# Performance work log

Measured on AMD Instinct MI355X. Metric: run time of the kernel, lower is better.

## Reference

```python
import jax, jax.numpy as jnp
import numpy as np


def conv2d_same(x, w, b=None):
    # x: [B,C,H,W], w: [O,I,kh,kw], stride 1, SAME padding (pad=1 for 3x3)
    out = jax.lax.conv_general_dilated(
        x, w, window_strides=(1, 1), padding='SAME',
        dimension_numbers=('NCHW', 'OIHW', 'NCHW'))
    if b is not None:
        out = out + b[None, :, None, None]
    return out


def deform_conv(x, offset, wd, k=3, pad=1, dg=4):
    # DCNv1: per-location offset-guided bilinear sampling + weighted accumulation.
    # x: [B,C,H,W]; offset: [B, dg*k*k*2, H, W] as (dy,dx) pairs per kernel tap;
    # wd: [O, C, k, k] (bias-free, as in mmcv DeformConv).
    B, C, H, W = x.shape
    cg = C // dg          # channels per deformable group
    K = k * k
    off = offset.reshape(B, dg, K, 2, H, W)
    dy, dx = off[:, :, :, 0], off[:, :, :, 1]          # [B,dg,K,H,W]
    ky = (jnp.arange(K) // k - pad).astype(x.dtype)    # kernel row offsets
    kx = (jnp.arange(K) % k - pad).astype(x.dtype)     # kernel col offsets
    hh = jnp.arange(H, dtype=x.dtype)
    ww = jnp.arange(W, dtype=x.dtype)
    py = dy + ky[None, None, :, None, None] + hh[None, None, None, :, None]
    px = dx + kx[None, None, :, None, None] + ww[None, None, None, None, :]
    y0 = jnp.floor(py); x0 = jnp.floor(px)
    wy1 = py - y0; wy0 = 1.0 - wy1
    wx1 = px - x0; wx0 = 1.0 - wx1
    xg = x.reshape(B, dg, cg, H * W)

    def gather(yi, xi):
        # zero outside the feature map (implicit zero padding of bilinear kernel)
        valid = (yi >= 0) & (yi < H) & (xi >= 0) & (xi < W)
        yc = jnp.clip(yi, 0, H - 1).astype(jnp.int32)
        xc = jnp.clip(xi, 0, W - 1).astype(jnp.int32)
        idx = (yc * W + xc).reshape(B, dg, 1, K * H * W)
        g = jnp.take_along_axis(xg, jnp.broadcast_to(idx, (B, dg, cg, K * H * W)), axis=-1)
        g = g.reshape(B, dg, cg, K, H, W)
        return g * valid[:, :, None].astype(x.dtype)

    val = (gather(y0, x0) * (wy0 * wx0)[:, :, None]
           + gather(y0, x0 + 1) * (wy0 * wx1)[:, :, None]
           + gather(y0 + 1, x0) * (wy1 * wx0)[:, :, None]
           + gather(y0 + 1, x0 + 1) * (wy1 * wx1)[:, :, None])  # [B,dg,cg,K,H,W]
    wr = wd.reshape(wd.shape[0], dg, cg, K)
    return jnp.einsum('ogck,bgckhw->bohw', wr, val)


def setup_inputs() -> dict:
    key = jax.random.key(0)
    k1, k2, k3, k4 = jax.random.split(key, 4)
    B, C, H, W = 8, 256, 64, 64
    dg, ks = 4, 3
    x = jax.random.normal(k1, (B, C, H, W), dtype=jnp.float32)
    w1 = jax.random.normal(k2, (C, C, 3, 3), dtype=jnp.float32) * 0.01
    b1 = jnp.zeros((C,), dtype=jnp.float32)
    w2 = jax.random.normal(k3, (dg * ks * ks * 2, C, 3, 3), dtype=jnp.float32) * 0.01
    b2 = jnp.zeros((dg * ks * ks * 2,), dtype=jnp.float32)
    wd = jax.random.normal(k4, (C, C, ks, ks), dtype=jnp.float32) * 0.01
    return {'x': x, 'w1': w1, 'b1': b1, 'w2': w2, 'b2': b2, 'wd': wd}


def reference(x, w1, b1, w2, b2, wd):
    # offset branch uses x.detach() in the original
    xd = jax.lax.stop_gradient(x)
    offset = conv2d_same(conv2d_same(xd, w1, b1), w2, b2)
    return jax.nn.relu(deform_conv(x, offset, wd, k=3, pad=1, dg=4))
```

## Files before the change

### kernel.cpp

```cpp
#include <hip/hip_runtime.h>
#include <hip/hip_bf16.h>


typedef __attribute__((ext_vector_type(8))) short bf16x8;
typedef __attribute__((ext_vector_type(4))) float f32x4;

static __device__ __forceinline__ ushort f2bf(float f) {
  __hip_bfloat16 h = __float2bfloat16(f);
  return *reinterpret_cast<ushort*>(&h);
}
static __device__ __forceinline__ float bf2f(ushort u) {
  union { uint u32; float f; } cv;
  cv.u32 = ((uint)u) << 16;
  return cv.f;
}

__global__ __launch_bounds__(256) void prep_weights(
    const float* __restrict__ w1, const float* __restrict__ w2,
    const float* __restrict__ wd,
    ushort* __restrict__ wt1b, ushort* __restrict__ wt2b,
    ushort* __restrict__ wtdb) {
  const int N1 = 256 * 2304, N2 = 128 * 2304, N3 = 256 * 2304;
  int total = N1 + N2 + N3;
  for (int i = blockIdx.x * 256 + threadIdx.x; i < total; i += gridDim.x * 256) {
    if (i < N1) {
      int co = i / 2304, r = i % 2304;
      int ti = r >> 6, cc = r & 63;
      int kk = ti >> 2, chunk = ti & 3;
      wt1b[i] = f2bf(w1[(co * 256 + chunk * 64 + cc) * 9 + kk]);
    } else if (i < N1 + N2) {
      int d = i - N1;
      int co = d / 2304, r = d % 2304;
      int ti = r >> 6, cc = r & 63;
      int kk = ti >> 2, chunk = ti & 3;
      wt2b[d] = (co < 72) ? f2bf(w2[(co * 256 + chunk * 64 + cc) * 9 + kk])
                          : (ushort)0;
    } else {
      int d = i - N1 - N2;
      int co = d / 2304, r = d % 2304;
      int ti = r >> 6, c = r & 63;
      int g = ti / 9, kk = ti - g * 9;
      wtdb[d] = f2bf(wd[(co * 256 + g * 64 + c) * 9 + kk]);
    }
  }
}

__global__ __launch_bounds__(256) void transpose_x(
    const float* __restrict__ x, ushort* __restrict__ xt) {
  int id = blockIdx.x;
  int y = id & 63, bg = id >> 6;
  int c = threadIdx.x & 63, xi = threadIdx.x >> 6;
  const float* ip = x + (((size_t)bg) << 18) + ((size_t)c << 12) + y * 64;
  ushort* op = xt + (((size_t)bg) << 18) + (size_t)y * 4096 + c;
#pragma unroll
  for (int j = 0; j < 16; ++j) {
    int xx = xi * 16 + j;
    op[(size_t)xx * 64] = f2bf(ip[xx]);
  }
}

template <int MODE, int NFR, int CO_TILE, bool RELU, bool HASBIAS, bool OUT_CHLAST>
__global__ __launch_bounds__(256, 2) void fa_mfma2(
    const ushort* __restrict__ inT,
    const float* __restrict__ off,
    const ushort* __restrict__ wB,
    const float* __restrict__ bias,
    void* __restrict__ outp,
    int co_total, int co_write) {
  constexpr int NCALLS = (CO_TILE * 144 + 4095) / 4096;
  constexpr int BUFN = NCALLS * 2048;
  __shared__ __align__(16) ushort Blds[2][BUFN];

  int id = blockIdx.x;
  int bh = (id & 7) * 64 + (id >> 3);
  int b = bh >> 6, h = bh & 63;
  int t = threadIdx.x;
  int wave = t >> 6, lane = t & 63;
  int ml = lane & 15, kc = lane >> 4;
  int px = wave * 16 + ml;

  int rb_i[NCALLS];
#pragma unroll
  for (int m = 0; m < NCALLS; ++m) {
    int dest = m * 4096 + t * 16;
    int co = dest / 144;
    int r = dest - co * 144;
    rb_i[m] = co * 4608 + (r >= 128 ? 0 : r);
  }
  const char* wBb = (const char*)wB;

  auto stage = [&](int ti, int bufsel) {
#pragma unroll
    for (int m = 0; m < NCALLS; ++m) {
      const void* src = (const void*)(wBb + (rb_i[m] + ti * 128));
      ushort* dst = &Blds[bufsel][m * 2048 + wave * 512];
      __builtin_amdgcn_global_load_lds(
          (const __attribute__((address_space(1))) void*)src,
          (__attribute__((address_space(3))) void*)dst, 16, 0, 0);
    }
  };

  f32x4 acc[NFR];
#pragma unroll
  for (int j = 0; j < NFR; ++j) acc[j] = (f32x4){0.f, 0.f, 0.f, 0.f};

  stage(0, 0);
  __syncthreads();

  for (int ti = 0; ti < 36; ++ti) {
    int cur = ti & 1;
    if (ti < 35) stage(ti + 1, cur ^ 1);

    bf16x8 a0, a1;
    if (MODE == 0) {
      int kk = ti >> 2, chunk = ti & 3;
      int ky = kk / 3, kx = kk - ky * 3;
      int gy = h + ky - 1, gx = px + kx - 1;
      bool inb = (gy >= 0) & (gy < 64) & (gx >= 0) & (gx < 64);
      const ushort* p =
          inT + ((((size_t)(b * 4 + chunk) << 12) + gy * 64 + gx) << 6) + kc * 8;
      bf16x8 z = {0, 0, 0, 0, 0, 0, 0, 0};
      a0 = inb ? *(const bf16x8*)p : z;
      a1 = inb ? *(const bf16x8*)(p + 32) : z;
    } else {
      int g = ti / 9, kk = ti - g * 9;
      int ky = kk / 3, kx = kk - ky * 3;
      const float* offp = off + (((size_t)b * 72 + g * 18 + kk * 2) << 12) + h * 64;
      float dy = offp[px];
      float dx = offp[4096 + px];
      float py = (float)(h + ky - 1) + dy;
      float pxf = (float)(px + kx - 1) + dx;
      float y0f = floorf(py), x0f = floorf(pxf);
      float wy1 = py - y0f, wx1 = pxf - x0f;
      float wy0 = 1.f - wy1, wx0 = 1.f - wx1;
      int y0 = (int)y0f, x0i = (int)x0f;
      int y1 = y0 + 1, x1i = x0i + 1;
      bool vy0 = (y0 >= 0) & (y0 < 64);
      bool vy1 = (y1 >= 0) & (y1 < 64);
      bool vx0 = (x0i >= 0) & (x0i < 64);
      bool vx1 = (x1i >= 0) & (x1i < 64);
      float w00 = (vy0 & vx0) ? wy0 * wx0 : 0.f;
      float w01 = (vy0 & vx1) ? wy0 * wx1 : 0.f;
      float w10 = (vy1 & vx0) ? wy1 * wx0 : 0.f;
      float w11 = (vy1 & vx1) ? wy1 * wx1 : 0.f;
      int yc0 = min(max(y0, 0), 63), yc1 = min(max(y1, 0), 63);
      int xc0 = min(max(x0i, 0), 63), xc1 = min(max(x1i, 0), 63);
      const ushort* base = inT + (((size_t)(b * 4 + g)) << 18) + kc * 8;
      const ushort* p00 = base + ((yc0 * 64 + xc0) << 6);
      const ushort* p01 = base + ((yc0 * 64 + xc1) << 6);
      const ushort* p10 = base + ((yc1 * 64 + xc0) << 6);
      const ushort* p11 = base + ((yc1 * 64 + xc1) << 6);
#pragma unroll
      for (int ks = 0; ks < 2; ++ks) {
        bf16x8 r00 = *(const bf16x8*)(p00 + ks * 32);
        bf16x8 r01 = *(const bf16x8*)(p01 + ks * 32);
        bf16x8 r10 = *(const bf16x8*)(p10 + ks * 32);
        bf16x8 r11 = *(const bf16x8*)(p11 + ks * 32);
        uint pk[4];
#pragma unroll
        for (int jj = 0; jj < 4; ++jj) {
          float v0 = w00 * bf2f((ushort)r00[2 * jj]) + w01 * bf2f((ushort)r01[2 * jj]) +
                     w10 * bf2f((ushort)r10[2 * jj]) + w11 * bf2f((ushort)r11[2 * jj]);
          float v1 = w00 * bf2f((ushort)r00[2 * jj + 1]) + w01 * bf2f((ushort)r01[2 * jj + 1]) +
                     w10 * bf2f((ushort)r10[2 * jj + 1]) + w11 * bf2f((ushort)r11[2 * jj + 1]);
          pk[jj] = (uint)f2bf(v0) | ((uint)f2bf(v1) << 16);
        }
        bf16x8 av;
        av[0] = (short)(pk[0] & 0xffff); av[1] = (short)(pk[0] >> 16);
        av[2] = (short)(pk[1] & 0xffff); av[3] = (short)(pk[1] >> 16);
        av[4] = (short)(pk[2] & 0xffff); av[5] = (short)(pk[2] >> 16);
        av[6] = (short)(pk[3] & 0xffff); av[7] = (short)(pk[3] >> 16);
        if (ks == 0) a0 = av; else a1 = av;
      }
    }

#pragma unroll
    for (int ks = 0; ks < 2; ++ks) {
      bf16x8 av = ks ? a1 : a0;
#pragma unroll
      for (int nf = 0; nf < NFR; ++nf) {
        bf16x8 bq = *(const bf16x8*)&Blds[cur][(nf * 16 + ml) * 72 + ks * 32 + kc * 8];
        acc[nf] = __builtin_amdgcn_mfma_f32_16x16x32_bf16(av, bq, acc[nf], 0, 0, 0);
      }
    }

    if (ti < 35) __syncthreads();
  }

  int rq = lane >> 4;
#pragma unroll
  for (int nf = 0; nf < NFR; ++nf) {
    int co = nf * 16 + ml;
    if (co < co_write) {
      float bv = HASBIAS ? bias[co] : 0.f;
      if (OUT_CHLAST) {
        int g_out = co >> 6, ci = co & 63;
        ushort* op = (ushort*)outp +
                     ((((size_t)(b * 4 + g_out) << 12) + h * 64) << 6) + ci;
#pragma unroll
        for (int ri = 0; ri < 4; ++ri) {
          int pxe = wave * 16 + rq * 4 + ri;
          float v = acc[nf][ri] + bv;
          if (RELU) v = fmaxf(v, 0.f);
          op[(size_t)pxe << 6] = f2bf(v);
        }
      } else {
        float* op = (float*)outp + (((size_t)b * co_total + co) << 12) + h * 64;
#pragma unroll
        for (int ri = 0; ri < 4; ++ri) {
          int pxe = wave * 16 + rq * 4 + ri;
          float v = acc[nf][ri] + bv;
          if (RELU) v = fmaxf(v, 0.f);
          op[pxe] = v;
        }
      }
    }
  }
}

extern "C" void kernel_launch(void* const* d_in, const int* in_sizes, int n_in,
                              void* d_out, int out_size, void* d_ws, size_t ws_size,
                              hipStream_t stream) {
  const float* x  = (const float*)d_in[0];
  const float* w1 = (const float*)d_in[1];
  const float* b1 = (const float*)d_in[2];
  const float* w2 = (const float*)d_in[3];
  const float* b2 = (const float*)d_in[4];
  const float* wd = (const float*)d_in[5];

  char* wsb = (char*)d_ws;
  float*  off_buf = (float*)wsb;
  ushort* xt      = (ushort*)(wsb + 9437184);
  ushort* wt1b    = (ushort*)(wsb + 26214400);
  ushort* wt2b    = (ushort*)(wsb + 27394048);
  ushort* wtdb    = (ushort*)(wsb + 27983872);

  prep_weights<<<2048, 256, 0, stream>>>(w1, w2, wd, wt1b, wt2b, wtdb);
  transpose_x<<<2048, 256, 0, stream>>>(x, xt);

  fa_mfma2<0, 16, 256, false, true, true>
      <<<512, 256, 0, stream>>>(xt, nullptr, wt1b, b1, d_out, 256, 256);

  fa_mfma2<0, 5, 80, false, true, false>
      <<<512, 256, 0, stream>>>((const ushort*)d_out, nullptr, wt2b, b2,
                                off_buf, 72, 72);

  fa_mfma2<1, 16, 256, true, false, false>
      <<<512, 256, 0, stream>>>(xt, off_buf, wtdb, nullptr, d_out, 256, 256);
}
```

Measured before the change: 209.0 us.

## Retile MFMA conv kernels with register-blocked M/N tiles and prefetched A operands

Generalizes the fused conv/deform-conv MFMA kernel so each wave computes several 16-pixel M fragments against a shared set of B fragments. Output channels can now be split across workgroups, and each workgroup can cover multiple image rows. The A-operand gathers (plain im2col loads, or offset reads plus the four bilinear corner loads) are issued one step ahead, so their latency overlaps the current step's MFMAs. The aim is more B-tile reuse from LDS and hidden gather latency, at the cost of higher register pressure and different occupancy per launch.

```diff
diff --git a/kernel.cpp b/kernel.cpp
--- a/kernel.cpp
+++ b/kernel.cpp
@@ -59,77 +59,118 @@
   }
 }
 
-template <int MODE, int NFR, int CO_TILE, bool RELU, bool HASBIAS, bool OUT_CHLAST>
-__global__ __launch_bounds__(256, 2) void fa_mfma2(
+template <int MODE, int MFR, int NFR, int NWAVES, int NSPLIT,
+          bool RELU, bool HASBIAS, bool OUT_CHLAST, int MINW>
+__global__ __launch_bounds__(NWAVES * 64, MINW) void fa_mfma3(
     const ushort* __restrict__ inT,
     const float* __restrict__ off,
     const ushort* __restrict__ wB,
     const float* __restrict__ bias,
     void* __restrict__ outp,
     int co_total, int co_write) {
-  constexpr int NCALLS = (CO_TILE * 144 + 4095) / 4096;
-  constexpr int BUFN = NCALLS * 2048;
+  constexpr int THREADS = NWAVES * 64;
+  constexpr int CO_TILE = NFR * 16;
+  constexpr int MB = NWAVES * MFR * 16;
+  constexpr int ROWS = MB / 64;
+  constexpr int NCALLS = (CO_TILE * 144 + THREADS * 16 - 1) / (THREADS * 16);
+  constexpr int BUFN = NCALLS * THREADS * 8;
+  constexpr int NRN = (MODE == 1) ? 8 : 2;
   __shared__ __align__(16) ushort Blds[2][BUFN];
 
+  const int nwg = 8 * (64 / ROWS) * NSPLIT;
   int id = blockIdx.x;
-  int bh = (id & 7) * 64 + (id >> 3);
-  int b = bh >> 6, h = bh & 63;
+  int id2 = (id & 7) * (nwg >> 3) + (id >> 3);
+  int coh = id2 % NSPLIT;
+  int rg = (id2 / NSPLIT) % (64 / ROWS);
+  int b = id2 / (NSPLIT * (64 / ROWS));
+  int h0 = rg * ROWS;
+  int co_base = coh * CO_TILE;
+
   int t = threadIdx.x;
-  int wave = t >> 6, lane = t & 63;
+  int wv = t >> 6, lane = t & 63;
   int ml = lane & 15, kc = lane >> 4;
-  int px = wave * 16 + ml;
+
+  const char* wBb = (const char*)(wB + (size_t)co_base * 2304);
 
   int rb_i[NCALLS];
 #pragma unroll
   for (int m = 0; m < NCALLS; ++m) {
-    int dest = m * 4096 + t * 16;
+    int dest = (m * THREADS + t) * 16;
     int co = dest / 144;
     int r = dest - co * 144;
+    if (co > CO_TILE - 1) co = CO_TILE - 1;
     rb_i[m] = co * 4608 + (r >= 128 ? 0 : r);
   }
-  const char* wBb = (const char*)wB;
 
   auto stage = [&](int ti, int bufsel) {
 #pragma unroll
     for (int m = 0; m < NCALLS; ++m) {
-      const void* src = (const void*)(wBb + (rb_i[m] + ti * 128));
-      ushort* dst = &Blds[bufsel][m * 2048 + wave * 512];
+      const void* src = (const void*)(wBb + ((size_t)rb_i[m] + ti * 128));
+      ushort* dst = &Blds[bufsel][(m * THREADS + t) * 8];
       __builtin_amdgcn_global_load_lds(
           (const __attribute__((address_space(1))) void*)src,
           (__attribute__((address_space(3))) void*)dst, 16, 0, 0);
     }
   };
 
-  f32x4 acc[NFR];
-#pragma unroll
-  for (int j = 0; j < NFR; ++j) acc[j] = (f32x4){0.f, 0.f, 0.f, 0.f};
-
-  stage(0, 0);
-  __syncthreads();
-
-  for (int ti = 0; ti < 36; ++ti) {
-    int cur = ti & 1;
-    if (ti < 35) stage(ti + 1, cur ^ 1);
-
-    bf16x8 a0, a1;
-    if (MODE == 0) {
-      int kk = ti >> 2, chunk = ti & 3;
-      int ky = kk / 3, kx = kk - ky * 3;
-      int gy = h + ky - 1, gx = px + kx - 1;
+  int prow[MFR], pcol[MFR];
+#pragma unroll
+  for (int mf = 0; mf < MFR; ++mf) {
+    int pxg = wv * MFR * 16 + mf * 16 + ml;
+    prow[mf] = h0 + (pxg >> 6);
+    pcol[mf] = pxg & 63;
+  }
+
+  const bf16x8 bz = {0, 0, 0, 0, 0, 0, 0, 0};
+  bf16x8 aCur[MFR][2];
+  bf16x8 rN[MFR][NRN];
+  float wsv[MFR][4];
+  float2 offA[MFR];
+
+  auto issueA0 = [&](int tn) {
+    int kk = tn >> 2, chunk = tn & 3;
+    int ky = kk / 3, kx = kk - ky * 3;
+#pragma unroll
+    for (int mf = 0; mf < MFR; ++mf) {
+      int gy = prow[mf] + ky - 1, gx = pcol[mf] + kx - 1;
       bool inb = (gy >= 0) & (gy < 64) & (gx >= 0) & (gx < 64);
       const ushort* p =
           inT + ((((size_t)(b * 4 + chunk) << 12) + gy * 64 + gx) << 6) + kc * 8;
-      bf16x8 z = {0, 0, 0, 0, 0, 0, 0, 0};
-      a0 = inb ? *(const bf16x8*)p : z;
-      a1 = inb ? *(const bf16x8*)(p + 32) : z;
-    } else {
-      int g = ti / 9, kk = ti - g * 9;
-      int ky = kk / 3, kx = kk - ky * 3;
-      const float* offp = off + (((size_t)b * 72 + g * 18 + kk * 2) << 12) + h * 64;
-      float dy = offp[px];
-      float dx = offp[4096 + px];
-      float py = (float)(h + ky - 1) + dy;
-      float pxf = (float)(px + kx - 1) + dx;
+      rN[mf][0] = bz;
+      rN[mf][1] = bz;
+      if (inb) {
+        rN[mf][0] = *(const bf16x8*)p;
+        rN[mf][1] = *(const bf16x8*)(p + 32);
+      }
+    }
+  };
+  auto finishA0 = [&]() {
+#pragma unroll
+    for (int mf = 0; mf < MFR; ++mf) {
+      aCur[mf][0] = rN[mf][0];
+      aCur[mf][1] = rN[mf][1];
+    }
+  };
+
+  auto loadOff = [&](int tn) {
+    int g = tn / 9, kk = tn - 9 * (tn / 9);
+    int ch = g * 18 + kk * 2;
+#pragma unroll
+    for (int mf = 0; mf < MFR; ++mf) {
+      const float* offp =
+          off + (((size_t)b * 72 + ch) << 12) + prow[mf] * 64 + pcol[mf];
+      offA[mf].x = offp[0];
+      offA[mf].y = offp[4096];
+    }
+  };
+  auto issueA1 = [&](int tn) {
+    int g = tn / 9, kk = tn - 9 * (tn / 9);
+    int ky = kk / 3, kx = kk - ky * 3;
+    const ushort* base = inT + (((size_t)(b * 4 + g)) << 18) + kc * 8;
+#pragma unroll
+    for (int mf = 0; mf < MFR; ++mf) {
+      float py = (float)(prow[mf] + ky - 1) + offA[mf].x;
+      float pxf = (float)(pcol[mf] + kx - 1) + offA[mf].y;
       float y0f = floorf(py), x0f = floorf(pxf);
       float wy1 = py - y0f, wx1 = pxf - x0f;
       float wy0 = 1.f - wy1, wx0 = 1.f - wx1;
@@ -139,79 +180,115 @@
       bool vy1 = (y1 >= 0) & (y1 < 64);
       bool vx0 = (x0i >= 0) & (x0i < 64);
       bool vx1 = (x1i >= 0) & (x1i < 64);
-      float w00 = (vy0 & vx0) ? wy0 * wx0 : 0.f;
-      float w01 = (vy0 & vx1) ? wy0 * wx1 : 0.f;
-      float w10 = (vy1 & vx0) ? wy1 * wx0 : 0.f;
-      float w11 = (vy1 & vx1) ? wy1 * wx1 : 0.f;
+      wsv[mf][0] = (vy0 & vx0) ? wy0 * wx0 : 0.f;
+      wsv[mf][1] = (vy0 & vx1) ? wy0 * wx1 : 0.f;
+      wsv[mf][2] = (vy1 & vx0) ? wy1 * wx0 : 0.f;
+      wsv[mf][3] = (vy1 & vx1) ? wy1 * wx1 : 0.f;
       int yc0 = min(max(y0, 0), 63), yc1 = min(max(y1, 0), 63);
       int xc0 = min(max(x0i, 0), 63), xc1 = min(max(x1i, 0), 63);
-      const ushort* base = inT + (((size_t)(b * 4 + g)) << 18) + kc * 8;
       const ushort* p00 = base + ((yc0 * 64 + xc0) << 6);
       const ushort* p01 = base + ((yc0 * 64 + xc1) << 6);
       const ushort* p10 = base + ((yc1 * 64 + xc0) << 6);
       const ushort* p11 = base + ((yc1 * 64 + xc1) << 6);
+      rN[mf][0] = *(const bf16x8*)p00;
+      rN[mf][1] = *(const bf16x8*)(p00 + 32);
+      rN[mf][2] = *(const bf16x8*)p01;
+      rN[mf][3] = *(const bf16x8*)(p01 + 32);
+      rN[mf][4] = *(const bf16x8*)p10;
+      rN[mf][5] = *(const bf16x8*)(p10 + 32);
+      rN[mf][6] = *(const bf16x8*)p11;
+      rN[mf][7] = *(const bf16x8*)(p11 + 32);
+    }
+  };
+  auto finishA1 = [&]() {
+#pragma unroll
+    for (int mf = 0; mf < MFR; ++mf) {
+      float w00 = wsv[mf][0], w01 = wsv[mf][1];
+      float w10 = wsv[mf][2], w11 = wsv[mf][3];
 #pragma unroll
       for (int ks = 0; ks < 2; ++ks) {
-        bf16x8 r00 = *(const bf16x8*)(p00 + ks * 32);
-        bf16x8 r01 = *(const bf16x8*)(p01 + ks * 32);
-        bf16x8 r10 = *(const bf16x8*)(p10 + ks * 32);
-        bf16x8 r11 = *(const bf16x8*)(p11 + ks * 32);
-        uint pk[4];
+        bf16x8 q00 = rN[mf][0 + ks], q01 = rN[mf][2 + ks];
+        bf16x8 q10 = rN[mf][4 + ks], q11 = rN[mf][6 + ks];
+        bf16x8 av;
 #pragma unroll
         for (int jj = 0; jj < 4; ++jj) {
-          float v0 = w00 * bf2f((ushort)r00[2 * jj]) + w01 * bf2f((ushort)r01[2 * jj]) +
-                     w10 * bf2f((ushort)r10[2 * jj]) + w11 * bf2f((ushort)r11[2 * jj]);
-          float v1 = w00 * bf2f((ushort)r00[2 * jj + 1]) + w01 * bf2f((ushort)r01[2 * jj + 1]) +
-                     w10 * bf2f((ushort)r10[2 * jj + 1]) + w11 * bf2f((ushort)r11[2 * jj + 1]);
-          pk[jj] = (uint)f2bf(v0) | ((uint)f2bf(v1) << 16);
+          float v0 = w00 * bf2f((ushort)q00[2 * jj]) + w01 * bf2f((ushort)q01[2 * jj]) +
+                     w10 * bf2f((ushort)q10[2 * jj]) + w11 * bf2f((ushort)q11[2 * jj]);
+          float v1 = w00 * bf2f((ushort)q00[2 * jj + 1]) + w01 * bf2f((ushort)q01[2 * jj + 1]) +
+                     w10 * bf2f((ushort)q10[2 * jj + 1]) + w11 * bf2f((ushort)q11[2 * jj + 1]);
+          av[2 * jj] = (short)f2bf(v0);
+          av[2 * jj + 1] = (short)f2bf(v1);
         }
-        bf16x8 av;
-        av[0] = (short)(pk[0] & 0xffff); av[1] = (short)(pk[0] >> 16);
-        av[2] = (short)(pk[1] & 0xffff); av[3] = (short)(pk[1] >> 16);
-        av[4] = (short)(pk[2] & 0xffff); av[5] = (short)(pk[2] >> 16);
-        av[6] = (short)(pk[3] & 0xffff); av[7] = (short)(pk[3] >> 16);
-        if (ks == 0) a0 = av; else a1 = av;
+        aCur[mf][ks] = av;
       }
     }
+  };
+
+  f32x4 acc[MFR][NFR];
+#pragma unroll
+  for (int i = 0; i < MFR; ++i)
+#pragma unroll
+    for (int j = 0; j < NFR; ++j) acc[i][j] = (f32x4){0.f, 0.f, 0.f, 0.f};
+
+  if (MODE == 1) {
+    loadOff(0);
+    issueA1(0);
+    loadOff(1);
+    finishA1();
+  } else {
+    issueA0(0);
+    finishA0();
+  }
+  stage(0, 0);
+  __syncthreads();
+
+  for (int ti = 0; ti < 36; ++ti) {
+    int cur = ti & 1;
+    if (ti < 35) {
+      stage(ti + 1, cur ^ 1);
+      if (MODE == 1) issueA1(ti + 1); else issueA0(ti + 1);
+    }
+    if (MODE == 1 && ti < 34) loadOff(ti + 2);
 
 #pragma unroll
     for (int ks = 0; ks < 2; ++ks) {
-      bf16x8 av = ks ? a1 : a0;
-#pragma unroll
-      for (int nf = 0; nf < NFR; ++nf) {
-        bf16x8 bq = *(const bf16x8*)&Blds[cur][(nf * 16 + ml) * 72 + ks * 32 + kc * 8];
-        acc[nf] = __builtin_amdgcn_mfma_f32_16x16x32_bf16(av, bq, acc[nf], 0, 0, 0);
-      }
-    }
-
-    if (ti < 35) __syncthreads();
+      bf16x8 bq[NFR];
+#pragma unroll
+      for (int nf = 0; nf < NFR; ++nf)
+        bq[nf] = *(const bf16x8*)&Blds[cur][(nf * 16 + ml) * 72 + ks * 32 + kc * 8];
+#pragma unroll
+      for (int mf = 0; mf < MFR; ++mf)
+#pragma unroll
+        for (int nf = 0; nf < NFR; ++nf)
+          acc[mf][nf] = __builtin_amdgcn_mfma_f32_16x16x32_bf16(
+              aCur[mf][ks], bq[nf], acc[mf][nf], 0, 0, 0);
+    }
+
+    if (ti < 35) { if (MODE == 1) finishA1(); else finishA0(); }
+    __syncthreads();
   }
 
   int rq = lane >> 4;
 #pragma unroll
   for (int nf = 0; nf < NFR; ++nf) {
-    int co = nf * 16 + ml;
-    if (co < co_write) {
-      float bv = HASBIAS ? bias[co] : 0.f;
-      if (OUT_CHLAST) {
-        int g_out = co >> 6, ci = co & 63;
-        ushort* op = (ushort*)outp +
-                     ((((size_t)(b * 4 + g_out) << 12) + h * 64) << 6) + ci;
+    int cog = co_base + nf * 16 + ml;
+    if (cog < co_write) {
+      float bv = HASBIAS ? bias[cog] : 0.f;
+#pragma unroll
+      for (int mf = 0; mf < MFR; ++mf) {
 #pragma unroll
         for (int ri = 0; ri < 4; ++ri) {
-          int pxe = wave * 16 + rq * 4 + ri;
-          float v = acc[nf][ri] + bv;
+          int pxe = wv * MFR * 16 + mf * 16 + rq * 4 + ri;
+          int row = h0 + (pxe >> 6), col = pxe & 63;
+          float v = acc[mf][nf][ri] + bv;
           if (RELU) v = fmaxf(v, 0.f);
-          op[(size_t)pxe << 6] = f2bf(v);
-        }
-      } else {
-        float* op = (float*)outp + (((size_t)b * co_total + co) << 12) + h * 64;
-#pragma unroll
-        for (int ri = 0; ri < 4; ++ri) {
-          int pxe = wave * 16 + rq * 4 + ri;
-          float v = acc[nf][ri] + bv;
-          if (RELU) v = fmaxf(v, 0.f);
-          op[pxe] = v;
+          if (OUT_CHLAST) {
+            int g_out = cog >> 6, ci = cog & 63;
+            ((ushort*)outp)[((((size_t)(b * 4 + g_out) << 12) + row * 64 + col) << 6) + ci] =
+                f2bf(v);
+          } else {
+            ((float*)outp)[(((size_t)b * co_total + cog) << 12) + row * 64 + col] = v;
+          }
         }
       }
     }
@@ -238,13 +315,13 @@
   prep_weights<<<2048, 256, 0, stream>>>(w1, w2, wd, wt1b, wt2b, wtdb);
   transpose_x<<<2048, 256, 0, stream>>>(x, xt);
 
-  fa_mfma2<0, 16, 256, false, true, true>
-      <<<512, 256, 0, stream>>>(xt, nullptr, wt1b, b1, d_out, 256, 256);
-
-  fa_mfma2<0, 5, 80, false, true, false>
-      <<<512, 256, 0, stream>>>((const ushort*)d_out, nullptr, wt2b, b2,
+  fa_mfma3<0, 4, 8, 2, 2, false, true, true, 1>
+      <<<512, 128, 0, stream>>>(xt, nullptr, wt1b, b1, d_out, 256, 256);
+
+  fa_mfma3<0, 2, 5, 2, 1, false, true, false, 2>
+      <<<512, 128, 0, stream>>>((const ushort*)d_out, nullptr, wt2b, b2,
                                 off_buf, 72, 72);
 
-  fa_mfma2<1, 16, 256, true, false, false>
+  fa_mfma3<1, 2, 8, 4, 2, true, false, false, 2>
       <<<512, 256, 0, stream>>>(xt, off_buf, wtdb, nullptr, d_out, 256, 256);
 }
```

Measured after the change: 243.8 us. +16.7%, slower.
